# Performance work log

Measured on AMD Instinct MI355X. Metric: run time of the kernel, lower is better.

Reference implementation:

```python
import jax, jax.numpy as jnp
import numpy as np

S, E, H, D, L = 2048, 1024, 16, 64, 6  # seq, embed(=H*D), heads, d_model, stack
FF = 4 * E
EPS = 1e-5


def _pos_embedding():
    pos = jnp.arange(S, dtype=jnp.float32)[:, None]
    idx = jnp.arange(E, dtype=jnp.float32)[None, :]
    ang = pos / jnp.power(10000.0, idx / E)
    # even positions -> sin row, odd positions -> cos row (as in the source)
    return jnp.where(jnp.arange(S)[:, None] % 2 == 0, jnp.sin(ang), jnp.cos(ang))


def _layer_norm(x, g, b):
    mu = jnp.mean(x, axis=-1, keepdims=True)
    var = jnp.mean(jnp.square(x - mu), axis=-1, keepdims=True)
    return (x - mu) * jax.lax.rsqrt(var + EPS) * g + b


def setup_inputs() -> dict:
    key = jax.random.key(0)
    ks = jax.random.split(key, 12)
    n = lambda k, shape, s=0.02: jax.random.normal(k, shape, jnp.float32) * s
    return {
        "x": jax.random.normal(ks[0], (S, E), jnp.float32),
        # shared (default-arg trap) input projections [d_model, embed]
        "Wk": n(ks[1], (D, E)), "Wq": n(ks[2], (D, E)), "Wv": n(ks[3], (D, E)),
        # per-layer per-head linears (stored [in,out])
        "hWk": n(ks[4], (L, H, D, D)), "hbk": jnp.zeros((L, H, D), jnp.float32),
        "hWq": n(ks[5], (L, H, D, D)), "hbq": jnp.zeros((L, H, D), jnp.float32),
        "hWv": n(ks[6], (L, H, D, D)), "hbv": jnp.zeros((L, H, D), jnp.float32),
        "Wo": n(ks[7], (L, E, E)), "bo": jnp.zeros((L, E), jnp.float32),
        "ln1_g": jnp.ones((L, E), jnp.float32), "ln1_b": jnp.zeros((L, E), jnp.float32),
        "W1": n(ks[8], (L, E, FF)), "b1": jnp.zeros((L, FF), jnp.float32),
        "W2": n(ks[9], (L, FF, E)), "b2": jnp.zeros((L, E), jnp.float32),
        "ln2_g": jnp.ones((L, E), jnp.float32), "ln2_b": jnp.zeros((L, E), jnp.float32),
    }


def reference(x, Wk, Wq, Wv, hWk, hbk, hWq, hbq, hWv, hbv, Wo, bo,
              ln1_g, ln1_b, W1, b1, W2, b2, ln2_g, ln2_b):
    h = x + _pos_embedding()
    scale = 1.0 / jnp.sqrt(jnp.float32(D))
    for l in range(L):
        # shared projections: [S, D]
        K = h @ Wk.T
        Q = h @ Wq.T
        V = h @ Wv.T
        # per-head linears: [H, S, D]
        kh = jnp.einsum('sd,hde->hse', K, hWk[l]) + hbk[l][:, None, :]
        qh = jnp.einsum('sd,hde->hse', Q, hWq[l]) + hbq[l][:, None, :]
        vh = jnp.einsum('sd,hde->hse', V, hWv[l]) + hbv[l][:, None, :]
        scores = jnp.einsum('hqd,hkd->hqk', qh, kh) * scale  # [H, S, S]
        attn = jax.nn.softmax(scores, axis=-1)
        out = jnp.einsum('hqk,hkd->hqd', attn, vh)           # [H, S, D]
        cat = jnp.transpose(out, (1, 0, 2)).reshape(S, H * D)  # [S, E]
        o = cat @ Wo[l] + bo[l]
        h = _layer_norm(o + h, ln1_g[l], ln1_b[l])
        # FFN
        f = jax.nn.relu(h @ W1[l] + b1[l]) @ W2[l] + b2[l]
        h = _layer_norm(f + h, ln2_g[l], ln2_b[l])
    return h
```

## Files before the change

kernel.cpp:

```cpp
#include <hip/hip_runtime.h>
#include <stdint.h>

typedef unsigned short u16;
typedef unsigned int   u32;

constexpr int SS = 2048, EE = 1024, HH = 16, DD = 64, LL = 6, FF = 4096;

typedef __bf16 bf16x8 __attribute__((ext_vector_type(8)));
typedef float  f32x4  __attribute__((ext_vector_type(4)));

#define DEV __device__ __forceinline__
#define AS1 __attribute__((address_space(1)))
#define AS3 __attribute__((address_space(3)))

DEV u16 f2bf(float f) {
    u32 u = __builtin_bit_cast(u32, f);
    u += 0x7FFFu + ((u >> 16) & 1u);
    return (u16)(u >> 16);
}

DEV float bf2f(u16 v) { return __builtin_bit_cast(float, (u32)v << 16); }

DEV void store_bf4(u16* p, float a, float b, float c, float d) {
    u32 lo = (u32)f2bf(a) | ((u32)f2bf(b) << 16);
    u32 hi = (u32)f2bf(c) | ((u32)f2bf(d) << 16);
    *(uint2*)p = make_uint2(lo, hi);
}

DEV void gload16(const void* g, void* l) {
    __builtin_amdgcn_global_load_lds((const AS1 void*)g, (AS3 void*)l, 16, 0, 0);
}

DEV f32x4 mfma16(bf16x8 a, bf16x8 b, f32x4 c) {
    return __builtin_amdgcn_mfma_f32_16x16x32_bf16(a, b, c, 0, 0, 0);
}

DEV float exp2_fast(float x) {
    float r;
    asm("v_exp_f32 %0, %1" : "=v"(r) : "v"(x));
    return r;
}

DEV int kvperm(int c) {
    return (c & 32) | ((c & 12) << 1) | ((c & 16) >> 2) | (c & 3);
}

DEV int xcd_swz(int flat, int nwg) {
    int chunk = nwg >> 3;
    return (flat & 7) * chunk + (flat >> 3);
}

constexpr size_t ALGN(size_t x) { return (x + 255) & ~(size_t)255; }
constexpr size_t OFF_WSHB = 0;
constexpr size_t OFF_HVB  = ALGN(OFF_WSHB + (size_t)3*64*1024*2);
constexpr size_t OFF_KQV3 = ALGN(OFF_HVB  + (size_t)96*4096*2);
constexpr size_t OFF_WVOT = ALGN(OFF_KQV3 + (size_t)3*SS*64*2);
constexpr size_t OFF_BO2  = ALGN(OFF_WVOT + (size_t)LL*EE*EE*2);
constexpr size_t OFF_HWT  = ALGN(OFF_BO2  + (size_t)LL*EE*4);
constexpr size_t OFF_HB   = ALGN(OFF_HWT  + (size_t)3*96*4096*2);
constexpr size_t OFF_WOT  = ALGN(OFF_HB   + (size_t)LL*3*HH*64*4);
constexpr size_t OFF_W1T  = ALGN(OFF_WOT  + (size_t)LL*EE*EE*2);
constexpr size_t OFF_W2T  = ALGN(OFF_W1T  + (size_t)LL*FF*EE*2);
constexpr size_t OFF_HBF  = ALGN(OFF_W2T  + (size_t)LL*EE*FF*2);
constexpr size_t OFF_QKVH = ALGN(OFF_HBF  + (size_t)SS*EE*2);
constexpr size_t OFF_VT   = OFF_QKVH + (size_t)2*HH*SS*64*2;
constexpr size_t OFF_CAT  = OFF_VT   + (size_t)64*SS*2;
constexpr size_t OFF_F1   = OFF_QKVH;
constexpr size_t OFF_OF   = ALGN(OFF_F1  + (size_t)SS*FF*2);

__global__ void pos_add(const float* __restrict__ x, u16* __restrict__ hb) {
    const int row = blockIdx.x, tid = threadIdx.x;
    float4 x4 = ((const float4*)(x + (size_t)row * EE))[tid];
    float v[4] = {x4.x, x4.y, x4.z, x4.w};
    float y[4];
#pragma unroll
    for (int j = 0; j < 4; ++j) {
        int e = tid * 4 + j;
        float ang = (float)row * expf((float)e * (-9.210340371976184f / 1024.f));
        float pe = ((row & 1) == 0) ? sinf(ang) : cosf(ang);
        y[j] = v[j] + pe;
    }
    store_bf4(hb + (size_t)row * EE + tid * 4, y[0], y[1], y[2], y[3]);
}

__global__ void pack_bias(const float* __restrict__ bk, const float* __restrict__ bq,
                          const float* __restrict__ bv, float* __restrict__ dst) {
    int i = blockIdx.x * 256 + threadIdx.x;
    if (i >= LL * 3 * HH * 64) return;
    int d = i & 63;
    int hh = (i >> 6) & 15;
    int lt = i >> 10;
    int t = lt % 3, l = lt / 3;
    const float* s = (t == 0) ? bk : (t == 1) ? bq : bv;
    dst[i] = s[((size_t)l * HH + hh) * 64 + d];
}

DEV void tile_t64(const float* src, u16* dst, int R, int C, int c0, int r0,
                  float (*t)[65], int tid) {
    const int lr = tid >> 4, lc4 = (tid & 15) * 4;
#pragma unroll
    for (int i = 0; i < 4; ++i) {
        int r = i * 16 + lr;
        float4 v = *(const float4*)(src + (size_t)(r0 + r) * C + c0 + lc4);
        t[r][lc4] = v.x; t[r][lc4 + 1] = v.y; t[r][lc4 + 2] = v.z; t[r][lc4 + 3] = v.w;
    }
    __syncthreads();
    const int cr = tid >> 3, rr8 = (tid & 7) * 8;
#pragma unroll
    for (int i = 0; i < 2; ++i) {
        int cc = i * 32 + cr;
        u16 tmp[8];
#pragma unroll
        for (int j = 0; j < 8; ++j) tmp[j] = f2bf(t[rr8 + j][cc]);
        *(uint4*)(dst + (size_t)(c0 + cc) * R + r0 + rr8) = *(uint4*)tmp;
    }
}

__global__ void transpose_cast64(const float* __restrict__ src, u16* __restrict__ dst,
                                 int R, int C, long sSrc, long sDst) {
    __shared__ float t[64][65];
    const int b = blockIdx.z;
    tile_t64(src + (size_t)b * sSrc, dst + (size_t)b * sDst, R, C,
             blockIdx.x * 64, blockIdx.y * 64, t, threadIdx.x);
}

__global__ void hw_t3(const float* __restrict__ s0, const float* __restrict__ s1,
                      const float* __restrict__ s2, u16* __restrict__ dst) {
    __shared__ float t[64][65];
    const int z = blockIdx.z;
    const float* src = (z < 96 ? s0 : z < 192 ? s1 : s2) + (size_t)(z % 96) * 4096;
    tile_t64(src, dst + (size_t)z * 4096, 64, 64, 0, 0, t, threadIdx.x);
}

__global__ void wsh_cast(const float* __restrict__ s0, const float* __restrict__ s1,
                         const float* __restrict__ s2, u16* __restrict__ dst) {
    const int z = blockIdx.z, row = blockIdx.x, tid = threadIdx.x;
    const float* s = (z == 0 ? s0 : z == 1 ? s1 : s2) + (size_t)row * 1024 + tid * 4;
    float4 v = *(const float4*)s;
    store_bf4(dst + ((size_t)z * 64 + row) * 1024 + tid * 4, v.x, v.y, v.z, v.w);
}

__global__ void hv_cast(const float* __restrict__ src, u16* __restrict__ dst) {
    size_t i = ((size_t)blockIdx.x * 256 + threadIdx.x) * 4;
    float4 v = *(const float4*)(src + i);
    store_bf4(dst + i, v.x, v.y, v.z, v.w);
}

__global__ void bo_fold(const float* __restrict__ bo, const float* __restrict__ hbv,
                        const float* __restrict__ Wo, float* __restrict__ BO2) {
    const int l = blockIdx.z, e = blockIdx.x * 256 + threadIdx.x;
    float acc = bo[(size_t)l * EE + e];
    const float* w = Wo + (size_t)l * EE * EE + e;
    const float* bv = hbv + (size_t)l * EE;
    for (int j = 0; j < EE; ++j) acc += bv[j] * w[(size_t)j * EE];
    BO2[(size_t)l * EE + e] = acc;
}

template<int BIASMODE, bool RELU, bool SPLITK, bool BATCH>
__launch_bounds__(256)
__global__ void gemm_std(const u16* __restrict__ A, const u16* __restrict__ B,
                         const float* __restrict__ bias, u16* __restrict__ Cb,
                         int M, int N, int K, int lda, int ldb,
                         long zsA, long zsB, long zsC) {
    __shared__ u16 As[2][128 * 64];
    __shared__ u16 Bs[2][128 * 64];
    const int gx = gridDim.x;
    const int swz = xcd_swz(blockIdx.y * gx + blockIdx.x, gx * gridDim.y);
    const int bn = swz % gx, bm = swz / gx, z = blockIdx.z;
    const int tid = threadIdx.x, w = tid >> 6;
    const int lane = tid & 63, l15 = lane & 15, hi = lane >> 4;
    const int wm = w >> 1, wn = w & 1;
    const u16* Ab = A + (size_t)bm * 128 * lda + (SPLITK ? (size_t)z * K : 0) + (BATCH ? (size_t)z * zsA : 0);
    const u16* Bb = B + (size_t)bn * 128 * ldb + (SPLITK ? (size_t)z * K : 0) + (BATCH ? (size_t)z * zsB : 0);
    const size_t coff = SPLITK ? (size_t)z * M * N : (BATCH ? (size_t)z * zsC : 0);
    const int tr = tid >> 3, tp = tid & 7;

    f32x4 acc[4][4];
#pragma unroll
    for (int i = 0; i < 4; ++i)
#pragma unroll
        for (int j = 0; j < 4; ++j) acc[i][j] = f32x4{0.f, 0.f, 0.f, 0.f};

    auto STAGE = [&](int b, int kt) {
        const u16* Abk = Ab + kt + (size_t)tr * lda + tp * 8;
        const u16* Bbk = Bb + kt + (size_t)tr * ldb + tp * 8;
#pragma unroll
        for (int i = 0; i < 4; ++i) {
            gload16(Abk + (size_t)i * 32 * lda, &As[b][(i * 256 + w * 64) * 8]);
            gload16(Bbk + (size_t)i * 32 * ldb, &Bs[b][(i * 256 + w * 64) * 8]);
        }
    };

    STAGE(0, 0);
    __syncthreads();
    int buf = 0;

    for (int kt = 0; kt < K; kt += 64) {
        if (kt + 64 < K) STAGE(buf ^ 1, kt + 64);
#pragma unroll
        for (int kk = 0; kk < 2; ++kk) {
            bf16x8 af[4], bf[4];
#pragma unroll
            for (int mi = 0; mi < 4; ++mi)
                af[mi] = *(const bf16x8*)&As[buf][(wm * 64 + mi * 16 + l15) * 64 + kk * 32 + hi * 8];
#pragma unroll
            for (int ni = 0; ni < 4; ++ni)
                bf[ni] = *(const bf16x8*)&Bs[buf][(wn * 64 + ni * 16 + l15) * 64 + kk * 32 + hi * 8];
#pragma unroll
            for (int mi = 0; mi < 4; ++mi)
#pragma unroll
                for (int ni = 0; ni < 4; ++ni)
                    acc[mi][ni] = mfma16(af[mi], bf[ni], acc[mi][ni]);
        }
        __syncthreads();
        buf ^= 1;
    }

#pragma unroll
    for (int mi = 0; mi < 4; ++mi) {
        int rg = bm * 128 + wm * 64 + mi * 16 + hi * 4;
#pragma unroll
        for (int ni = 0; ni < 4; ++ni) {
            int cg = bn * 128 + wn * 64 + ni * 16 + l15;
            float bc = (BIASMODE == 1) ? bias[cg] : 0.f;
#pragma unroll
            for (int r = 0; r < 4; ++r) {
                float v = acc[mi][ni][r] + bc;
                if (RELU) v = fmaxf(v, 0.f);
                Cb[coff + (size_t)(rg + r) * N + cg] = f2bf(v);
            }
        }
    }
}

template<int EPI>
__launch_bounds__(256)
__global__ void gemm_small(const u16* __restrict__ A, const u16* __restrict__ B,
                           const float* __restrict__ bias, u16* __restrict__ C0,
                           u16* __restrict__ C1,
                           int K, int lda, int ldb, int ldc, int zdiv,
                           long aL, long aS, long bL, long bS, long cL, long cS) {
    __shared__ u16 As[2][64 * 64];
    __shared__ u16 Bs[2][64 * 64];
    const int bm = blockIdx.x, z = blockIdx.z;
    const int zq = z / zdiv, zr = z % zdiv;
    const int tid = threadIdx.x, w = tid >> 6;
    const int lane = tid & 63, l15 = lane & 15, hi = lane >> 4;
    const int wm = w >> 1, wn = w & 1;
    const u16* Ab = A + (size_t)bm * 64 * lda + (size_t)zq * aL + (size_t)zr * aS;
    const u16* Bb = B + (size_t)zq * bL + (size_t)zr * bS;
    const int tr = tid >> 3, tp = tid & 7;

    f32x4 acc[2][2];
#pragma unroll
    for (int i = 0; i < 2; ++i)
#pragma unroll
        for (int j = 0; j < 2; ++j) acc[i][j] = f32x4{0.f, 0.f, 0.f, 0.f};

    auto STAGE = [&](int b, int kt) {
        const u16* Abk = Ab + kt + (size_t)tr * lda + tp * 8;
        const u16* Bbk = Bb + kt + (size_t)tr * ldb + tp * 8;
#pragma unroll
        for (int i = 0; i < 2; ++i) {
            gload16(Abk + (size_t)i * 32 * lda, &As[b][(i * 256 + tid) * 8]);
            gload16(Bbk + (size_t)i * 32 * ldb, &Bs[b][(i * 256 + tid) * 8]);
        }
    };

    STAGE(0, 0);
    __syncthreads();
    int buf = 0;

    for (int kt = 0; kt < K; kt += 64) {
        if (kt + 64 < K) STAGE(buf ^ 1, kt + 64);
#pragma unroll
        for (int kk = 0; kk < 2; ++kk) {
            bf16x8 af[2], bf[2];
#pragma unroll
            for (int mi = 0; mi < 2; ++mi)
                af[mi] = *(const bf16x8*)&As[buf][(wm * 32 + mi * 16 + l15) * 64 + kk * 32 + hi * 8];
#pragma unroll
            for (int ni = 0; ni < 2; ++ni)
                bf[ni] = *(const bf16x8*)&Bs[buf][(wn * 32 + ni * 16 + l15) * 64 + kk * 32 + hi * 8];
#pragma unroll
            for (int mi = 0; mi < 2; ++mi)
#pragma unroll
                for (int ni = 0; ni < 2; ++ni)
                    acc[mi][ni] = mfma16(af[mi], bf[ni], acc[mi][ni]);
        }
        __syncthreads();
        buf ^= 1;
    }

#pragma unroll
    for (int mi = 0; mi < 2; ++mi) {
        const int rg = bm * 64 + wm * 32 + mi * 16 + hi * 4;
#pragma unroll
        for (int ni = 0; ni < 2; ++ni) {
            const int cn = wn * 32 + ni * 16 + l15;
            if (EPI == 0) {
#pragma unroll
                for (int r = 0; r < 4; ++r)
                    C0[(size_t)zq * cL + (size_t)zr * cS + (size_t)(rg + r) * ldc + cn] =
                        f2bf(acc[mi][ni][r]);
            } else if (EPI == 1) {
                const float sc = (z >= 16) ? 0.18033688011112042f : 1.f;
                const float bv = bias[z * 64 + cn];
                u16* dst = C0 + ((size_t)z * SS + rg) * 64 + cn;
#pragma unroll
                for (int r = 0; r < 4; ++r)
                    dst[(size_t)r * 64] = f2bf((acc[mi][ni][r] + bv) * sc);
            } else {
                if (z < 2) {
#pragma unroll
                    for (int r = 0; r < 4; ++r)
                        C0[(size_t)z * SS * 64 + (size_t)(rg + r) * 64 + cn] = f2bf(acc[mi][ni][r]);
                } else {
                    const int ps = (rg & ~63) | kvperm(rg & 63);
                    u16 tmp[4];
#pragma unroll
                    for (int r = 0; r < 4; ++r) tmp[r] = f2bf(acc[mi][ni][r]);
                    *(uint2*)(C1 + (size_t)cn * SS + ps) = *(uint2*)tmp;
                }
            }
        }
    }
}

__launch_bounds__(256)
__global__ void attn_fwd(const u16* __restrict__ QKVH, const u16* __restrict__ VT,
                         u16* __restrict__ cat) {
    const int logical = (blockIdx.x & 7) * 64 + (blockIdx.x >> 3);
    const int h = logical >> 5, qt = logical & 31;
    const int tid = threadIdx.x, w = tid >> 6, lane = tid & 63;
    const int l15 = lane & 15, hi = lane >> 4;
    __shared__ __align__(16) u16 smem[33824];

    const u16* qb = QKVH + (((size_t)(16 + h) * SS) + qt * 64) * 64;
    const u16* kb = QKVH + ((size_t)h * SS) * 64;
    const u16* vb = VT;

    bf16x8 bq[4][2];
#pragma unroll
    for (int qg = 0; qg < 4; ++qg) {
        bq[qg][0] = *(const bf16x8*)(qb + (qg * 16 + l15) * 64 + hi * 8);
        bq[qg][1] = *(const bf16x8*)(qb + (qg * 16 + l15) * 64 + 32 + hi * 8);
    }
    bf16x8 ONES;
#pragma unroll
    for (int i = 0; i < 8; ++i) ONES[i] = (__bf16)1.0f;

    f32x4 oacc[4][4];
#pragma unroll
    for (int i = 0; i < 4; ++i)
#pragma unroll
        for (int j = 0; j < 4; ++j) oacc[i][j] = f32x4{0.f, 0.f, 0.f, 0.f};
    f32x4 sacc[4];
#pragma unroll
    for (int i = 0; i < 4; ++i) sacc[i] = f32x4{0.f, 0.f, 0.f, 0.f};
    float mrun = 0.f;

    auto STAGE = [&](int buf, int t) {
#pragma unroll
        for (int j = 0; j < 4; ++j) {
            int fl = j * 256 + tid;
            int kr = fl >> 3, kc = (fl & 7) ^ (kr & 7);
            gload16(kb + ((size_t)(t * 128 + kr)) * 64 + kc * 8, smem + buf * 8192 + fl * 8);
            int vr = fl >> 4, vc = (fl & 15) ^ (vr & 7);
            gload16(vb + (size_t)vr * SS + t * 128 + vc * 8, smem + 16384 + buf * 8192 + fl * 8);
        }
    };

    STAGE(0, 0);
    __syncthreads();
    int buf = 0;
    const int kbase = w * 32;

    for (int t = 0; t < SS / 128; ++t) {
        if (t < SS / 128 - 1) STAGE(buf ^ 1, t + 1);
        const u16* ks = smem + buf * 8192;
        const u16* vs = smem + 16384 + buf * 8192;

        bf16x8 kf[2][2];
#pragma unroll
        for (int kvg = 0; kvg < 2; ++kvg) {
            int row = kbase + kvg * 16 + l15;
            const u16* kr = ks + row * 64;
            kf[kvg][0] = *(const bf16x8*)&kr[((0 * 4 + hi) ^ (row & 7)) * 8];
            kf[kvg][1] = *(const bf16x8*)&kr[((1 * 4 + hi) ^ (row & 7)) * 8];
        }

        f32x4 sc[4][2];
        __builtin_amdgcn_s_setprio(1);
#pragma unroll
        for (int qg = 0; qg < 4; ++qg)
#pragma unroll
            for (int kvg = 0; kvg < 2; ++kvg) {
                f32x4 a = f32x4{0.f, 0.f, 0.f, 0.f};
                a = mfma16(kf[kvg][0], bq[qg][0], a);
                a = mfma16(kf[kvg][1], bq[qg][1], a);
                sc[qg][kvg] = a;
            }
        __builtin_amdgcn_s_setprio(0);

        bf16x8 pa[4];
#pragma unroll
        for (int qg = 0; qg < 4; ++qg) {
            bf16x8 v;
#pragma unroll
            for (int r = 0; r < 4; ++r) {
                v[r]     = (__bf16)exp2_fast(sc[qg][0][r] - mrun);
                v[4 + r] = (__bf16)exp2_fast(sc[qg][1][r] - mrun);
            }
            pa[qg] = v;
        }

        bf16x8 bv[4];
#pragma unroll
        for (int di = 0; di < 4; ++di) {
            int d = di * 16 + l15;
            bv[di] = *(const bf16x8*)&vs[d * 128 + (((w * 4 + hi) ^ (d & 7)) * 8)];
        }

        __builtin_amdgcn_s_setprio(1);
#pragma unroll
        for (int qg = 0; qg < 4; ++qg) {
            sacc[qg] = mfma16(pa[qg], ONES, sacc[qg]);
#pragma unroll
            for (int di = 0; di < 4; ++di)
                oacc[qg][di] = mfma16(pa[qg], bv[di], oacc[qg][di]);
        }
        __builtin_amdgcn_s_setprio(0);

        float mx = sacc[0][0];
#pragma unroll
        for (int qg = 0; qg < 4; ++qg)
#pragma unroll
            for (int r = 0; r < 4; ++r) mx = fmaxf(mx, sacc[qg][r]);
        if (__any(mx > 1.0e30f)) {
            const float dn = 5.421010862427522e-20f;
            mrun += 64.f;
#pragma unroll
            for (int qg = 0; qg < 4; ++qg) {
#pragma unroll
                for (int r = 0; r < 4; ++r) sacc[qg][r] *= dn;
#pragma unroll
                for (int di = 0; di < 4; ++di)
#pragma unroll
                    for (int r = 0; r < 4; ++r) oacc[qg][di][r] *= dn;
            }
        }

        __syncthreads();
        buf ^= 1;
    }

    float* P4   = (float*)smem;
    float* sred = P4 + 4 * 64 * 65;
    float* smr  = sred + 4 * 64;
#pragma unroll
    for (int qg = 0; qg < 4; ++qg) {
        int q = qg * 16 + hi * 4;
#pragma unroll
        for (int di = 0; di < 4; ++di)
#pragma unroll
            for (int r = 0; r < 4; ++r)
                P4[(size_t)(w * 64 + q + r) * 65 + di * 16 + l15] = oacc[qg][di][r];
        if (l15 == 0) {
#pragma unroll
            for (int r = 0; r < 4; ++r) sred[w * 64 + q + r] = sacc[qg][r];
        }
    }
    if (lane == 0) smr[w] = mrun;
    __syncthreads();

    float mmax = fmaxf(fmaxf(smr[0], smr[1]), fmaxf(smr[2], smr[3]));
    float wsc[4];
#pragma unroll
    for (int sw = 0; sw < 4; ++sw) wsc[sw] = exp2_fast(smr[sw] - mmax);

    float rs[4];
#pragma unroll
    for (int r = 0; r < 4; ++r) {
        int q = w * 16 + hi * 4 + r;
        float s = 0.f;
#pragma unroll
        for (int sw = 0; sw < 4; ++sw) s += sred[sw * 64 + q] * wsc[sw];
        rs[r] = 1.f / s;
    }
#pragma unroll
    for (int di = 0; di < 4; ++di) {
        int col = h * 64 + di * 16 + l15;
#pragma unroll
        for (int r = 0; r < 4; ++r) {
            int q = w * 16 + hi * 4 + r;
            float o = 0.f;
#pragma unroll
            for (int sw = 0; sw < 4; ++sw)
                o += P4[(size_t)(sw * 64 + q) * 65 + di * 16 + l15] * wsc[sw];
            cat[(size_t)(qt * 64 + q) * EE + col] = f2bf(o * rs[r]);
        }
    }
}

template<bool FINAL>
__launch_bounds__(256)
__global__ void add_ln4(const u16* __restrict__ o, const float* __restrict__ ob,
                        const u16* __restrict__ res,
                        const float* __restrict__ g, const float* __restrict__ b,
                        float* __restrict__ fout, u16* __restrict__ hb) {
    const int row = blockIdx.x, tid = threadIdx.x;
    const int w = tid >> 6, lane = tid & 63;
    float x0, x1, x2, x3;
    {
        ushort4 r4 = ((const ushort4*)(res + (size_t)row * EE))[tid];
        float4 ob4 = ((const float4*)ob)[tid];
        x0 = bf2f(r4.x) + ob4.x; x1 = bf2f(r4.y) + ob4.y;
        x2 = bf2f(r4.z) + ob4.z; x3 = bf2f(r4.w) + ob4.w;
    }
#pragma unroll
    for (int z = 0; z < 4; ++z) {
        ushort4 a4 = ((const ushort4*)(o + (size_t)z * SS * EE + (size_t)row * EE))[tid];
        x0 += bf2f(a4.x); x1 += bf2f(a4.y); x2 += bf2f(a4.z); x3 += bf2f(a4.w);
    }
    float s = x0 + x1 + x2 + x3;
    float q = x0 * x0 + x1 * x1 + x2 * x2 + x3 * x3;
#pragma unroll
    for (int off = 1; off < 64; off <<= 1) { s += __shfl_xor(s, off); q += __shfl_xor(q, off); }
    __shared__ float red[8];
    if (lane == 0) { red[w] = s; red[4 + w] = q; }
    __syncthreads();
    s = red[0] + red[1] + red[2] + red[3];
    q = red[4] + red[5] + red[6] + red[7];
    const float mu = s * (1.f / EE);
    const float var = q * (1.f / EE) - mu * mu;
    const float rstd = rsqrtf(var + 1e-5f);
    const int c0 = tid * 4;
    float y0 = (x0 - mu) * rstd * g[c0 + 0] + b[c0 + 0];
    float y1 = (x1 - mu) * rstd * g[c0 + 1] + b[c0 + 1];
    float y2 = (x2 - mu) * rstd * g[c0 + 2] + b[c0 + 2];
    float y3 = (x3 - mu) * rstd * g[c0 + 3] + b[c0 + 3];
    if (FINAL) ((float4*)(fout + (size_t)row * EE))[tid] = make_float4(y0, y1, y2, y3);
    store_bf4(hb + (size_t)row * EE + c0, y0, y1, y2, y3);
}

extern "C" void kernel_launch(void* const* d_in, const int* in_sizes, int n_in,
                              void* d_out, int out_size, void* d_ws, size_t ws_size,
                              hipStream_t stream) {
    const float* x    = (const float*)d_in[0];
    const float* Wk   = (const float*)d_in[1];
    const float* Wq   = (const float*)d_in[2];
    const float* Wv   = (const float*)d_in[3];
    const float* hWk  = (const float*)d_in[4];
    const float* hbk  = (const float*)d_in[5];
    const float* hWq  = (const float*)d_in[6];
    const float* hbq  = (const float*)d_in[7];
    const float* hWv  = (const float*)d_in[8];
    const float* hbv  = (const float*)d_in[9];
    const float* Wo   = (const float*)d_in[10];
    const float* bo   = (const float*)d_in[11];
    const float* ln1g = (const float*)d_in[12];
    const float* ln1b = (const float*)d_in[13];
    const float* W1   = (const float*)d_in[14];
    const float* b1   = (const float*)d_in[15];
    const float* W2   = (const float*)d_in[16];
    const float* b2   = (const float*)d_in[17];
    const float* ln2g = (const float*)d_in[18];
    const float* ln2b = (const float*)d_in[19];

    char* ws = (char*)d_ws;
    u16*   WSHB = (u16*)(ws + OFF_WSHB);
    u16*   HVB  = (u16*)(ws + OFF_HVB);
    u16*   KQV3 = (u16*)(ws + OFF_KQV3);
    u16*   WVOT = (u16*)(ws + OFF_WVOT);
    float* BO2  = (float*)(ws + OFF_BO2);
    u16*   HWT  = (u16*)(ws + OFF_HWT);
    float* HB   = (float*)(ws + OFF_HB);
    u16*   WOT  = (u16*)(ws + OFF_WOT);
    u16*   W1T  = (u16*)(ws + OFF_W1T);
    u16*   W2T  = (u16*)(ws + OFF_W2T);
    u16*   HBF  = (u16*)(ws + OFF_HBF);
    u16*   QKVH = (u16*)(ws + OFF_QKVH);
    u16*   VT   = (u16*)(ws + OFF_VT);
    u16*   CAT  = (u16*)(ws + OFF_CAT);
    u16*   F1   = (u16*)(ws + OFF_F1);
    u16*   OFb  = (u16*)(ws + OFF_OF);

    pos_add<<<SS, 256, 0, stream>>>(x, HBF);
    pack_bias<<<72, 256, 0, stream>>>(hbk, hbq, hbv, HB);
    hw_t3<<<dim3(1, 1, 192), 256, 0, stream>>>(hWk, hWq, hWv, HWT);
    wsh_cast<<<dim3(64, 1, 3), 256, 0, stream>>>(Wk, Wq, Wv, WSHB);
    hv_cast<<<384, 256, 0, stream>>>(hWv, HVB);
    bo_fold<<<dim3(4, 1, LL), 256, 0, stream>>>(bo, hbv, Wo, BO2);
    transpose_cast64<<<dim3(16, 16, LL), 256, 0, stream>>>(Wo, WOT, EE, EE, (long)EE * EE, (long)EE * EE);
    transpose_cast64<<<dim3(64, 16, LL), 256, 0, stream>>>(W1, W1T, EE, FF, (long)EE * FF, (long)FF * EE);
    transpose_cast64<<<dim3(16, 64, LL), 256, 0, stream>>>(W2, W2T, FF, EE, (long)FF * EE, (long)EE * FF);
    gemm_small<0><<<dim3(16, 1, 96), 256, 0, stream>>>(
        WOT, HVB, nullptr, WVOT, nullptr, 64, 1024, 64, 1024, 16,
        (long)EE * EE, 64, (long)16 * 4096, 4096, (long)EE * EE, 64);

    for (int l = 0; l < LL; ++l) {
        gemm_small<3><<<dim3(32, 1, 3), 256, 0, stream>>>(
            HBF, WSHB, nullptr, KQV3, VT, 1024, 1024, 1024, 64, 64,
            0, 0, 0, (long)64 * 1024, 0, 0);
        gemm_small<1><<<dim3(32, 1, 32), 256, 0, stream>>>(
            KQV3, HWT + (size_t)l * 16 * 4096, HB + (size_t)l * 3072, QKVH, nullptr,
            64, 64, 64, 64, 16,
            (long)SS * 64, 0, (long)96 * 4096, 4096, 0, 0);

        attn_fwd<<<512, 256, 0, stream>>>(QKVH, VT, CAT);

        gemm_std<0, false, true, false><<<dim3(8, 16, 4), 256, 0, stream>>>(
            CAT, WVOT + (size_t)l * EE * EE, nullptr, OFb, SS, EE, 256, 1024, 1024, 0, 0, 0);
        add_ln4<false><<<SS, 256, 0, stream>>>(OFb, BO2 + (size_t)l * EE, HBF,
                                               ln1g + (size_t)l * EE, ln1b + (size_t)l * EE,
                                               nullptr, HBF);

        gemm_std<1, true, false, false><<<dim3(32, 16, 1), 256, 0, stream>>>(
            HBF, W1T + (size_t)l * FF * EE, b1 + (size_t)l * FF, F1, SS, FF, 1024, 1024, 1024, 0, 0, 0);
        gemm_std<0, false, true, false><<<dim3(8, 16, 4), 256, 0, stream>>>(
            F1, W2T + (size_t)l * EE * FF, nullptr, OFb, SS, EE, 1024, 4096, 4096, 0, 0, 0);
        if (l == LL - 1)
            add_ln4<true><<<SS, 256, 0, stream>>>(OFb, b2 + (size_t)l * EE, HBF,
                                                  ln2g + (size_t)l * EE, ln2b + (size_t)l * EE,
                                                  (float*)d_out, HBF);
        else
            add_ln4<false><<<SS, 256, 0, stream>>>(OFb, b2 + (size_t)l * EE, HBF,
                                                   ln2g + (size_t)l * EE, ln2b + (size_t)l * EE,
                                                   nullptr, HBF);
    }
}
```

Measured before the change: 917.3 us.

## Shrink attention query tile to 32 rows and load K/V directly from global

The attention kernel now handles 32 query rows per block instead of 64 and launches twice as many blocks. The LDS double-buffered K/V staging and per-iteration barrier are removed, so each wave reads its K and V fragments straight from global memory or cache. The epilogue is reworked so each thread writes 8 contiguous bf16 outputs with one vector store. The aim is more parallelism, less register and LDS pressure, and no barrier stalls, at the cost of more global traffic because K/V tiles are no longer shared through LDS and are reloaded by twice as many blocks.

```diff
diff --git a/kernel.cpp b/kernel.cpp
--- a/kernel.cpp
+++ b/kernel.cpp
@@ -330,19 +330,19 @@
 __launch_bounds__(256)
 __global__ void attn_fwd(const u16* __restrict__ QKVH, const u16* __restrict__ VT,
                          u16* __restrict__ cat) {
-    const int logical = (blockIdx.x & 7) * 64 + (blockIdx.x >> 3);
-    const int h = logical >> 5, qt = logical & 31;
+    const int logical = (blockIdx.x & 7) * 128 + (blockIdx.x >> 3);
+    const int h = logical >> 6, qt = logical & 63;
     const int tid = threadIdx.x, w = tid >> 6, lane = tid & 63;
     const int l15 = lane & 15, hi = lane >> 4;
-    __shared__ __align__(16) u16 smem[33824];
-
-    const u16* qb = QKVH + (((size_t)(16 + h) * SS) + qt * 64) * 64;
+    __shared__ __align__(16) float epi[4 * 32 * 65 + 4 * 32 + 4];
+
+    const u16* qb = QKVH + (((size_t)(16 + h) * SS) + qt * 32) * 64;
     const u16* kb = QKVH + ((size_t)h * SS) * 64;
     const u16* vb = VT;
 
-    bf16x8 bq[4][2];
-#pragma unroll
-    for (int qg = 0; qg < 4; ++qg) {
+    bf16x8 bq[2][2];
+#pragma unroll
+    for (int qg = 0; qg < 2; ++qg) {
         bq[qg][0] = *(const bf16x8*)(qb + (qg * 16 + l15) * 64 + hi * 8);
         bq[qg][1] = *(const bf16x8*)(qb + (qg * 16 + l15) * 64 + 32 + hi * 8);
     }
@@ -350,50 +350,33 @@
 #pragma unroll
     for (int i = 0; i < 8; ++i) ONES[i] = (__bf16)1.0f;
 
-    f32x4 oacc[4][4];
-#pragma unroll
-    for (int i = 0; i < 4; ++i)
+    f32x4 oacc[2][4];
+#pragma unroll
+    for (int i = 0; i < 2; ++i)
 #pragma unroll
         for (int j = 0; j < 4; ++j) oacc[i][j] = f32x4{0.f, 0.f, 0.f, 0.f};
-    f32x4 sacc[4];
-#pragma unroll
-    for (int i = 0; i < 4; ++i) sacc[i] = f32x4{0.f, 0.f, 0.f, 0.f};
+    f32x4 sacc[2];
+#pragma unroll
+    for (int i = 0; i < 2; ++i) sacc[i] = f32x4{0.f, 0.f, 0.f, 0.f};
     float mrun = 0.f;
 
-    auto STAGE = [&](int buf, int t) {
-#pragma unroll
-        for (int j = 0; j < 4; ++j) {
-            int fl = j * 256 + tid;
-            int kr = fl >> 3, kc = (fl & 7) ^ (kr & 7);
-            gload16(kb + ((size_t)(t * 128 + kr)) * 64 + kc * 8, smem + buf * 8192 + fl * 8);
-            int vr = fl >> 4, vc = (fl & 15) ^ (vr & 7);
-            gload16(vb + (size_t)vr * SS + t * 128 + vc * 8, smem + 16384 + buf * 8192 + fl * 8);
-        }
-    };
-
-    STAGE(0, 0);
-    __syncthreads();
-    int buf = 0;
     const int kbase = w * 32;
+    const u16* krow0 = kb + (size_t)(kbase + l15) * 64;
+    const u16* vrow0 = vb + (size_t)l15 * SS + (w * 4 + hi) * 8;
 
     for (int t = 0; t < SS / 128; ++t) {
-        if (t < SS / 128 - 1) STAGE(buf ^ 1, t + 1);
-        const u16* ks = smem + buf * 8192;
-        const u16* vs = smem + 16384 + buf * 8192;
-
         bf16x8 kf[2][2];
 #pragma unroll
         for (int kvg = 0; kvg < 2; ++kvg) {
-            int row = kbase + kvg * 16 + l15;
-            const u16* kr = ks + row * 64;
-            kf[kvg][0] = *(const bf16x8*)&kr[((0 * 4 + hi) ^ (row & 7)) * 8];
-            kf[kvg][1] = *(const bf16x8*)&kr[((1 * 4 + hi) ^ (row & 7)) * 8];
-        }
-
-        f32x4 sc[4][2];
+            const u16* kr = krow0 + (size_t)(t * 128 + kvg * 16) * 64;
+            kf[kvg][0] = *(const bf16x8*)(kr + hi * 8);
+            kf[kvg][1] = *(const bf16x8*)(kr + 32 + hi * 8);
+        }
+
+        f32x4 sc[2][2];
         __builtin_amdgcn_s_setprio(1);
 #pragma unroll
-        for (int qg = 0; qg < 4; ++qg)
+        for (int qg = 0; qg < 2; ++qg)
 #pragma unroll
             for (int kvg = 0; kvg < 2; ++kvg) {
                 f32x4 a = f32x4{0.f, 0.f, 0.f, 0.f};
@@ -403,9 +386,14 @@
             }
         __builtin_amdgcn_s_setprio(0);
 
-        bf16x8 pa[4];
-#pragma unroll
-        for (int qg = 0; qg < 4; ++qg) {
+        bf16x8 bv[4];
+#pragma unroll
+        for (int di = 0; di < 4; ++di)
+            bv[di] = *(const bf16x8*)(vrow0 + (size_t)di * 16 * SS + t * 128);
+
+        bf16x8 pa[2];
+#pragma unroll
+        for (int qg = 0; qg < 2; ++qg) {
             bf16x8 v;
 #pragma unroll
             for (int r = 0; r < 4; ++r) {
@@ -415,16 +403,9 @@
             pa[qg] = v;
         }
 
-        bf16x8 bv[4];
-#pragma unroll
-        for (int di = 0; di < 4; ++di) {
-            int d = di * 16 + l15;
-            bv[di] = *(const bf16x8*)&vs[d * 128 + (((w * 4 + hi) ^ (d & 7)) * 8)];
-        }
-
         __builtin_amdgcn_s_setprio(1);
 #pragma unroll
-        for (int qg = 0; qg < 4; ++qg) {
+        for (int qg = 0; qg < 2; ++qg) {
             sacc[qg] = mfma16(pa[qg], ONES, sacc[qg]);
 #pragma unroll
             for (int di = 0; di < 4; ++di)
@@ -432,16 +413,14 @@
         }
         __builtin_amdgcn_s_setprio(0);
 
-        float mx = sacc[0][0];
-#pragma unroll
-        for (int qg = 0; qg < 4; ++qg)
-#pragma unroll
-            for (int r = 0; r < 4; ++r) mx = fmaxf(mx, sacc[qg][r]);
+        float mx = fmaxf(fmaxf(sacc[0][0], sacc[0][1]), fmaxf(sacc[0][2], sacc[0][3]));
+#pragma unroll
+        for (int r = 0; r < 4; ++r) mx = fmaxf(mx, sacc[1][r]);
         if (__any(mx > 1.0e30f)) {
             const float dn = 5.421010862427522e-20f;
             mrun += 64.f;
 #pragma unroll
-            for (int qg = 0; qg < 4; ++qg) {
+            for (int qg = 0; qg < 2; ++qg) {
 #pragma unroll
                 for (int r = 0; r < 4; ++r) sacc[qg][r] *= dn;
 #pragma unroll
@@ -450,57 +429,47 @@
                     for (int r = 0; r < 4; ++r) oacc[qg][di][r] *= dn;
             }
         }
-
-        __syncthreads();
-        buf ^= 1;
-    }
-
-    float* P4   = (float*)smem;
-    float* sred = P4 + 4 * 64 * 65;
-    float* smr  = sred + 4 * 64;
-#pragma unroll
-    for (int qg = 0; qg < 4; ++qg) {
+    }
+
+    float* P4   = epi;
+    float* sred = epi + 4 * 32 * 65;
+    float* smr  = sred + 4 * 32;
+#pragma unroll
+    for (int qg = 0; qg < 2; ++qg) {
         int q = qg * 16 + hi * 4;
 #pragma unroll
         for (int di = 0; di < 4; ++di)
 #pragma unroll
             for (int r = 0; r < 4; ++r)
-                P4[(size_t)(w * 64 + q + r) * 65 + di * 16 + l15] = oacc[qg][di][r];
+                P4[(size_t)(w * 32 + q + r) * 65 + di * 16 + l15] = oacc[qg][di][r];
         if (l15 == 0) {
 #pragma unroll
-            for (int r = 0; r < 4; ++r) sred[w * 64 + q + r] = sacc[qg][r];
+            for (int r = 0; r < 4; ++r) sred[w * 32 + q + r] = sacc[qg][r];
         }
     }
     if (lane == 0) smr[w] = mrun;
     __syncthreads();
 
-    float mmax = fmaxf(fmaxf(smr[0], smr[1]), fmaxf(smr[2], smr[3]));
+    const float mmax = fmaxf(fmaxf(smr[0], smr[1]), fmaxf(smr[2], smr[3]));
     float wsc[4];
 #pragma unroll
     for (int sw = 0; sw < 4; ++sw) wsc[sw] = exp2_fast(smr[sw] - mmax);
 
-    float rs[4];
-#pragma unroll
-    for (int r = 0; r < 4; ++r) {
-        int q = w * 16 + hi * 4 + r;
-        float s = 0.f;
-#pragma unroll
-        for (int sw = 0; sw < 4; ++sw) s += sred[sw * 64 + q] * wsc[sw];
-        rs[r] = 1.f / s;
-    }
-#pragma unroll
-    for (int di = 0; di < 4; ++di) {
-        int col = h * 64 + di * 16 + l15;
-#pragma unroll
-        for (int r = 0; r < 4; ++r) {
-            int q = w * 16 + hi * 4 + r;
-            float o = 0.f;
-#pragma unroll
-            for (int sw = 0; sw < 4; ++sw)
-                o += P4[(size_t)(sw * 64 + q) * 65 + di * 16 + l15] * wsc[sw];
-            cat[(size_t)(qt * 64 + q) * EE + col] = f2bf(o * rs[r]);
-        }
-    }
+    const int row = tid >> 3, c0 = (tid & 7) * 8;
+    float s = 0.f;
+#pragma unroll
+    for (int sw = 0; sw < 4; ++sw) s += sred[sw * 32 + row] * wsc[sw];
+    const float rs = 1.f / s;
+    u16 outv[8];
+#pragma unroll
+    for (int j = 0; j < 8; ++j) {
+        float o = 0.f;
+#pragma unroll
+        for (int sw = 0; sw < 4; ++sw)
+            o += P4[(size_t)(sw * 32 + row) * 65 + c0 + j] * wsc[sw];
+        outv[j] = f2bf(o * rs);
+    }
+    *(uint4*)(cat + (size_t)(qt * 32 + row) * EE + h * 64 + c0) = *(uint4*)outv;
 }
 
 template<bool FINAL>
@@ -608,7 +577,7 @@
             64, 64, 64, 64, 16,
             (long)SS * 64, 0, (long)96 * 4096, 4096, 0, 0);
 
-        attn_fwd<<<512, 256, 0, stream>>>(QKVH, VT, CAT);
+        attn_fwd<<<1024, 256, 0, stream>>>(QKVH, VT, CAT);
 
         gemm_std<0, false, true, false><<<dim3(8, 16, 4), 256, 0, stream>>>(
             CAT, WVOT + (size_t)l * EE * EE, nullptr, OFb, SS, EE, 256, 1024, 1024, 0, 0, 0);
```

After: 1.119 ms. 1.22x slower.

## Load V fragments directly from global and shrink attention LDS footprint

Applied to the files above, without the earlier changes.

The attention kernel no longer stages V tiles through shared memory. Each lane now reads its V^T fragments straight from global memory every iteration, which halves the double-buffered LDS usage and may allow more resident blocks per CU. The epilogue is also restructured to reduce the per-wave partial outputs one 16-row group at a time in a smaller LDS buffer, writing 4 packed bf16 values per thread instead of scalar stores. The trade-off is direct global loads of V sitting in the inner loop, whose latency is less hidden than with async staging, plus extra barriers in the epilogue.

```diff
diff --git a/kernel.cpp b/kernel.cpp
--- a/kernel.cpp
+++ b/kernel.cpp
@@ -334,7 +334,9 @@
     const int h = logical >> 5, qt = logical & 31;
     const int tid = threadIdx.x, w = tid >> 6, lane = tid & 63;
     const int l15 = lane & 15, hi = lane >> 4;
-    __shared__ __align__(16) u16 smem[33824];
+    __shared__ __align__(16) u16 Ks[2][128 * 64];
+    __shared__ float sred[4 * 64];
+    __shared__ float smr[4];
 
     const u16* qb = QKVH + (((size_t)(16 + h) * SS) + qt * 64) * 64;
     const u16* kb = QKVH + ((size_t)h * SS) * 64;
@@ -365,9 +367,7 @@
         for (int j = 0; j < 4; ++j) {
             int fl = j * 256 + tid;
             int kr = fl >> 3, kc = (fl & 7) ^ (kr & 7);
-            gload16(kb + ((size_t)(t * 128 + kr)) * 64 + kc * 8, smem + buf * 8192 + fl * 8);
-            int vr = fl >> 4, vc = (fl & 15) ^ (vr & 7);
-            gload16(vb + (size_t)vr * SS + t * 128 + vc * 8, smem + 16384 + buf * 8192 + fl * 8);
+            gload16(kb + ((size_t)(t * 128 + kr)) * 64 + kc * 8, Ks[buf] + fl * 8);
         }
     };
 
@@ -375,12 +375,17 @@
     __syncthreads();
     int buf = 0;
     const int kbase = w * 32;
+    const u16* vrow0 = vb + (size_t)l15 * SS + (w * 4 + hi) * 8;
 
     for (int t = 0; t < SS / 128; ++t) {
         if (t < SS / 128 - 1) STAGE(buf ^ 1, t + 1);
-        const u16* ks = smem + buf * 8192;
-        const u16* vs = smem + 16384 + buf * 8192;
-
+
+        bf16x8 bv[4];
+#pragma unroll
+        for (int di = 0; di < 4; ++di)
+            bv[di] = *(const bf16x8*)(vrow0 + (size_t)di * 16 * SS + t * 128);
+
+        const u16* ks = Ks[buf];
         bf16x8 kf[2][2];
 #pragma unroll
         for (int kvg = 0; kvg < 2; ++kvg) {
@@ -415,13 +420,6 @@
             pa[qg] = v;
         }
 
-        bf16x8 bv[4];
-#pragma unroll
-        for (int di = 0; di < 4; ++di) {
-            int d = di * 16 + l15;
-            bv[di] = *(const bf16x8*)&vs[d * 128 + (((w * 4 + hi) ^ (d & 7)) * 8)];
-        }
-
         __builtin_amdgcn_s_setprio(1);
 #pragma unroll
         for (int qg = 0; qg < 4; ++qg) {
@@ -455,51 +453,46 @@
         buf ^= 1;
     }
 
-    float* P4   = (float*)smem;
-    float* sred = P4 + 4 * 64 * 65;
-    float* smr  = sred + 4 * 64;
 #pragma unroll
     for (int qg = 0; qg < 4; ++qg) {
-        int q = qg * 16 + hi * 4;
-#pragma unroll
-        for (int di = 0; di < 4; ++di)
-#pragma unroll
-            for (int r = 0; r < 4; ++r)
-                P4[(size_t)(w * 64 + q + r) * 65 + di * 16 + l15] = oacc[qg][di][r];
         if (l15 == 0) {
 #pragma unroll
-            for (int r = 0; r < 4; ++r) sred[w * 64 + q + r] = sacc[qg][r];
+            for (int r = 0; r < 4; ++r) sred[w * 64 + qg * 16 + hi * 4 + r] = sacc[qg][r];
         }
     }
     if (lane == 0) smr[w] = mrun;
     __syncthreads();
 
-    float mmax = fmaxf(fmaxf(smr[0], smr[1]), fmaxf(smr[2], smr[3]));
+    const float mmax = fmaxf(fmaxf(smr[0], smr[1]), fmaxf(smr[2], smr[3]));
     float wsc[4];
 #pragma unroll
     for (int sw = 0; sw < 4; ++sw) wsc[sw] = exp2_fast(smr[sw] - mmax);
 
-    float rs[4];
-#pragma unroll
-    for (int r = 0; r < 4; ++r) {
-        int q = w * 16 + hi * 4 + r;
+    float* P4c = (float*)Ks;
+    const int orow = tid >> 4, oc4 = (tid & 15) * 4;
+#pragma unroll 1
+    for (int qg = 0; qg < 4; ++qg) {
+#pragma unroll
+        for (int di = 0; di < 4; ++di)
+#pragma unroll
+            for (int r = 0; r < 4; ++r)
+                P4c[(size_t)(w * 16 + hi * 4 + r) * 66 + di * 16 + l15] = oacc[qg][di][r];
+        __syncthreads();
         float s = 0.f;
 #pragma unroll
-        for (int sw = 0; sw < 4; ++sw) s += sred[sw * 64 + q] * wsc[sw];
-        rs[r] = 1.f / s;
-    }
-#pragma unroll
-    for (int di = 0; di < 4; ++di) {
-        int col = h * 64 + di * 16 + l15;
-#pragma unroll
-        for (int r = 0; r < 4; ++r) {
-            int q = w * 16 + hi * 4 + r;
+        for (int sw = 0; sw < 4; ++sw) s += sred[sw * 64 + qg * 16 + orow] * wsc[sw];
+        const float rs = 1.f / s;
+        u16 ov[4];
+#pragma unroll
+        for (int j = 0; j < 4; ++j) {
             float o = 0.f;
 #pragma unroll
             for (int sw = 0; sw < 4; ++sw)
-                o += P4[(size_t)(sw * 64 + q) * 65 + di * 16 + l15] * wsc[sw];
-            cat[(size_t)(qt * 64 + q) * EE + col] = f2bf(o * rs[r]);
-        }
+                o += P4c[(size_t)(sw * 16 + orow) * 66 + oc4 + j] * wsc[sw];
+            ov[j] = f2bf(o * rs);
+        }
+        *(uint2*)(cat + (size_t)(qt * 64 + qg * 16 + orow) * EE + h * 64 + oc4) = *(uint2*)ov;
+        __syncthreads();
     }
 }
 
```

Result: slower. 1.311 ms (+42.9%).
